# Performance work log

Measured on AMD Instinct MI355X. Metric: run time of the kernel, lower is better.

## Reference

```python
import jax, jax.numpy as jnp
import numpy as np

T, B, D_IN, NQ = 256, 2048, 128, 8  # time, batch, input_dim, n_qubits == hidden_dim


def setup_inputs() -> dict:
    key = jax.random.key(0)
    ks = jax.random.split(key, 13)
    s = 1.0 / np.sqrt(D_IN + NQ)
    def lin(ka, kb):
        W = jax.random.uniform(ka, (D_IN + NQ, NQ), jnp.float32, -s, s)
        b = jax.random.uniform(kb, (NQ,), jnp.float32, -s, s)
        return W, b
    Wf, bf = lin(ks[0], ks[1])
    Wi, bi = lin(ks[2], ks[3])
    Wg, bg = lin(ks[4], ks[5])
    Wo, bo = lin(ks[6], ks[7])
    # trainable RX angles per wire for each of the 4 quantum gates
    thf = jax.random.normal(ks[8], (NQ,), jnp.float32) * 0.1
    thi = jax.random.normal(ks[9], (NQ,), jnp.float32) * 0.1
    thg = jax.random.normal(ks[10], (NQ,), jnp.float32) * 0.1
    tho = jax.random.normal(ks[11], (NQ,), jnp.float32) * 0.1
    inputs = jax.random.normal(ks[12], (T, B, D_IN), jnp.float32)
    return {"inputs": inputs, "Wf": Wf, "bf": bf, "Wi": Wi, "bi": bi,
            "Wg": Wg, "bg": bg, "Wo": Wo, "bo": bo,
            "thf": thf, "thi": thi, "thg": thg, "tho": tho}


def _qgate(lin_out, theta):
    # |0..0> -> RX(x_i) encode -> RX(theta_i) trainable -> <PauliZ_i> = cos(x_i + theta_i)
    return jnp.cos(lin_out + theta)


def reference(inputs, Wf, bf, Wi, bi, Wg, bg, Wo, bo, thf, thi, thg, tho):
    Bsz = inputs.shape[1]
    h0 = jnp.zeros((Bsz, NQ), inputs.dtype)
    c0 = jnp.zeros((Bsz, NQ), inputs.dtype)

    def step(carry, x):
        hx, cx = carry
        comb = jnp.concatenate([x, hx], axis=1)  # [B, D_IN+NQ]
        f = jax.nn.sigmoid(_qgate(comb @ Wf + bf, thf))
        i = jax.nn.sigmoid(_qgate(comb @ Wi + bi, thi))
        g = jnp.tanh(_qgate(comb @ Wg + bg, thg))
        o = jax.nn.sigmoid(_qgate(comb @ Wo + bo, tho))
        cx = f * cx + i * g
        hx = o * jnp.tanh(cx)
        return (hx, cx), hx

    (hx, cx), outputs = jax.lax.scan(step, (h0, c0), inputs)
    return outputs, hx, cx
```

## Files before the change

### kernel.cpp

```cpp
#include <hip/hip_runtime.h>

#define T_DIM 256
#define B_DIM 2048
#define D_IN_DIM 128
#define NQ 8
#define ROWS_PER_BLK 64
#define XSTRIDE 129
#define TSTRIDE 33

__global__ __launch_bounds__(256) void qlstm_gemm(
    const float* __restrict__ X,
    const float* __restrict__ Wf, const float* __restrict__ Wi,
    const float* __restrict__ Wg, const float* __restrict__ Wo,
    const float* __restrict__ bf, const float* __restrict__ bi,
    const float* __restrict__ bg, const float* __restrict__ bo,
    const float* __restrict__ thf, const float* __restrict__ thi,
    const float* __restrict__ thg, const float* __restrict__ tho,
    float4* __restrict__ Z)
{
    __shared__ float xs[ROWS_PER_BLK * XSTRIDE];
    __shared__ float wsh[4 * D_IN_DIM * NQ];

    const int t = (int)threadIdx.x;
    const int r0 = (int)blockIdx.x * ROWS_PER_BLK;

    const int wid  = __builtin_amdgcn_readfirstlane(t >> 6);
    const int lane = t & 63;

    const float* W  = (wid == 0) ? Wf  : (wid == 1) ? Wi  : (wid == 2) ? Wg  : Wo;
    const float* BB = (wid == 0) ? bf  : (wid == 1) ? bi  : (wid == 2) ? bg  : bo;
    const float* TH = (wid == 0) ? thf : (wid == 1) ? thi : (wid == 2) ? thg : tho;

    {
        const float4* Wg4 = (const float4*)W;
        float4* wd = (float4*)&wsh[wid * (D_IN_DIM * NQ)];
#pragma unroll
        for (int j = 0; j < 4; j++) wd[j * 64 + lane] = Wg4[j * 64 + lane];
    }

    const float4* Xg = (const float4*)(X + (size_t)r0 * D_IN_DIM);
#pragma unroll
    for (int i = 0; i < 8; i++) {
        int L = t + i * 256;
        float4 v = Xg[L];
        int row = L >> 5;
        int k4  = L & 31;
        float* d = &xs[row * XSTRIDE + k4 * 4];
        d[0] = v.x; d[1] = v.y; d[2] = v.z; d[3] = v.w;
    }
    __syncthreads();

    float acc[NQ];
#pragma unroll
    for (int q = 0; q < NQ; q++) acc[q] = BB[q] + TH[q];

    const float*  xrow = &xs[lane * XSTRIDE];
    const float4* wk   = (const float4*)&wsh[wid * (D_IN_DIM * NQ)];
#pragma unroll 4
    for (int k = 0; k < D_IN_DIM; k++) {
        float xk = xrow[k];
        float4 wa = wk[2 * k];
        float4 wb = wk[2 * k + 1];
        acc[0] += xk * wa.x; acc[1] += xk * wa.y; acc[2] += xk * wa.z; acc[3] += xk * wa.w;
        acc[4] += xk * wb.x; acc[5] += xk * wb.y; acc[6] += xk * wb.z; acc[7] += xk * wb.w;
    }

    __syncthreads();
    float* tile = xs;
#pragma unroll
    for (int q = 0; q < NQ; q++)
        tile[lane * TSTRIDE + q * 4 + wid] = acc[q];
    __syncthreads();

    float4* Zblk = Z + (size_t)r0 * NQ;
#pragma unroll
    for (int i = 0; i < 2; i++) {
        int F = t + i * 256;
        int r = F >> 3, q = F & 7;
        const float* s = &tile[r * TSTRIDE + q * 4];
        Zblk[F] = make_float4(s[0], s[1], s[2], s[3]);
    }
}

#define INV_2PI 0.15915494309189535f
#define L2E     1.4426950408889634f

__device__ __forceinline__ float hw_cos(float x) {
    return __builtin_amdgcn_cosf(x * INV_2PI);
}
__device__ __forceinline__ float hw_tanh(float x) {
    return 1.0f - 2.0f * __builtin_amdgcn_rcpf(__builtin_amdgcn_exp2f((2.0f * L2E) * x) + 1.0f);
}

#define POLY_G(u) \
    fmaf((u), fmaf((u), fmaf((u), -0.027717f, 0.120472f), -0.331065f), 0.999904f)

#define BCAST8(x, J) \
    __int_as_float(__builtin_amdgcn_ds_swizzle(__float_as_int(x), ((J) << 5) | 0x18))

#define LSTM_STEP_R(zv, hdst) { \
    float h0 = BCAST8(h, 0), h1 = BCAST8(h, 1), h2 = BCAST8(h, 2), h3 = BCAST8(h, 3); \
    float h4 = BCAST8(h, 4), h5 = BCAST8(h, 5), h6 = BCAST8(h, 6), h7 = BCAST8(h, 7); \
    float f0 = fmaf(h0, whf[0], (zv).x), f1 = fmaf(h1, whf[1], 0.0f); \
    float i0 = fmaf(h0, whi[0], (zv).y), i1 = fmaf(h1, whi[1], 0.0f); \
    float g0 = fmaf(h0, whg[0], (zv).z), g1 = fmaf(h1, whg[1], 0.0f); \
    float o0 = fmaf(h0, who[0], (zv).w), o1 = fmaf(h1, who[1], 0.0f); \
    f0 = fmaf(h2, whf[2], f0); f1 = fmaf(h3, whf[3], f1); \
    i0 = fmaf(h2, whi[2], i0); i1 = fmaf(h3, whi[3], i1); \
    g0 = fmaf(h2, whg[2], g0); g1 = fmaf(h3, whg[3], g1); \
    o0 = fmaf(h2, who[2], o0); o1 = fmaf(h3, who[3], o1); \
    f0 = fmaf(h4, whf[4], f0); f1 = fmaf(h5, whf[5], f1); \
    i0 = fmaf(h4, whi[4], i0); i1 = fmaf(h5, whi[5], i1); \
    g0 = fmaf(h4, whg[4], g0); g1 = fmaf(h5, whg[5], g1); \
    o0 = fmaf(h4, who[4], o0); o1 = fmaf(h5, who[5], o1); \
    f0 = fmaf(h6, whf[6], f0); f1 = fmaf(h7, whf[7], f1); \
    i0 = fmaf(h6, whi[6], i0); i1 = fmaf(h7, whi[7], i1); \
    g0 = fmaf(h6, whg[6], g0); g1 = fmaf(h7, whg[7], g1); \
    o0 = fmaf(h6, who[6], o0); o1 = fmaf(h7, who[7], o1); \
    float tf = hw_cos(f0 + f1); \
    float ti = hw_cos(i0 + i1); \
    float tg = hw_cos(g0 + g1); \
    float to = hw_cos(o0 + o1); \
    float pf = POLY_G(0.25f * (tf * tf)); \
    float pi_ = POLY_G(0.25f * (ti * ti)); \
    float pg = POLY_G(tg * tg); \
    float po = POLY_G(0.25f * (to * to)); \
    float fg = fmaf(tf * pf, 0.25f, 0.5f); \
    float ig = fmaf(ti * pi_, 0.25f, 0.5f); \
    float gg = tg * pg; \
    float og = fmaf(to * po, 0.25f, 0.5f); \
    c = fmaf(fg, c, ig * gg); \
    h = og * hw_tanh(c); \
    (hdst) = h; }

__global__ __launch_bounds__(64) void qlstm_recur(
    const float4* __restrict__ Z,
    const float* __restrict__ Wf, const float* __restrict__ Wi,
    const float* __restrict__ Wg, const float* __restrict__ Wo,
    float* __restrict__ out,
    float* __restrict__ state,
    int t0, int ct, int first, int last)
{
    const int tid = (int)blockIdx.x * 64 + (int)threadIdx.x;
    const int q   = tid & 7;

    float whf[8], whi[8], whg[8], who[8];
#pragma unroll
    for (int j = 0; j < 8; j++) {
        whf[j] = Wf[(D_IN_DIM + j) * NQ + q];
        whi[j] = Wi[(D_IN_DIM + j) * NQ + q];
        whg[j] = Wg[(D_IN_DIM + j) * NQ + q];
        who[j] = Wo[(D_IN_DIM + j) * NQ + q];
    }

    float h, c;
    if (first) { h = 0.0f; c = 0.0f; }
    else       { h = state[tid]; c = state[B_DIM * NQ + tid]; }

    const size_t stepsz = (size_t)B_DIM * NQ;
    const float4* Zp = Z + tid;
    float* og_ptr = out + (size_t)t0 * stepsz + tid;

    float4 bufA[8], bufB[8];
    float houtA[8], houtB[8];
#pragma unroll
    for (int s = 0; s < 8; s++) bufA[s] = Zp[(size_t)s * stepsz];

    for (int tb = 0; tb < ct; tb += 16) {
#pragma unroll
        for (int s = 0; s < 8; s++) bufB[s] = Zp[(size_t)(tb + 8 + s) * stepsz];
        __builtin_amdgcn_sched_barrier(0);
#pragma unroll
        for (int s = 0; s < 8; s++) {
            float4 z = bufA[s];
            LSTM_STEP_R(z, houtA[s])
        }
        if (tb + 16 < ct) {
#pragma unroll
            for (int s = 0; s < 8; s++) bufA[s] = Zp[(size_t)(tb + 16 + s) * stepsz];
        }
        __builtin_amdgcn_sched_barrier(0);
#pragma unroll
        for (int s = 0; s < 8; s++) og_ptr[(size_t)s * stepsz] = houtA[s];
#pragma unroll
        for (int s = 0; s < 8; s++) {
            float4 z = bufB[s];
            LSTM_STEP_R(z, houtB[s])
        }
#pragma unroll
        for (int s = 0; s < 8; s++) og_ptr[(size_t)(8 + s) * stepsz] = houtB[s];
        og_ptr += (size_t)16 * stepsz;
    }

    if (last) {
        out[(size_t)T_DIM * stepsz + tid] = h;
        out[(size_t)T_DIM * stepsz + stepsz + tid] = c;
    } else {
        state[tid] = h;
        state[B_DIM * NQ + tid] = c;
    }
}

extern "C" void kernel_launch(void* const* d_in, const int* in_sizes, int n_in,
                              void* d_out, int out_size, void* d_ws, size_t ws_size,
                              hipStream_t stream) {
    const float* X   = (const float*)d_in[0];
    const float* Wf  = (const float*)d_in[1];
    const float* bf  = (const float*)d_in[2];
    const float* Wi  = (const float*)d_in[3];
    const float* bi  = (const float*)d_in[4];
    const float* Wg  = (const float*)d_in[5];
    const float* bg  = (const float*)d_in[6];
    const float* Wo  = (const float*)d_in[7];
    const float* bo  = (const float*)d_in[8];
    const float* thf = (const float*)d_in[9];
    const float* thi = (const float*)d_in[10];
    const float* thg = (const float*)d_in[11];
    const float* tho = (const float*)d_in[12];
    float* out = (float*)d_out;

    const size_t state_bytes = (size_t)2 * B_DIM * NQ * sizeof(float);
    float* state = (float*)d_ws;
    float4* Zbuf = (float4*)((char*)d_ws + state_bytes);
    size_t avail = ws_size > state_bytes ? ws_size - state_bytes : 0;
    const size_t z_bytes_per_t = (size_t)B_DIM * NQ * sizeof(float4);
    int maxChunkT = (int)(avail / z_bytes_per_t);
    if (maxChunkT > T_DIM) maxChunkT = T_DIM;
    maxChunkT &= ~15;
    if (maxChunkT < 16) maxChunkT = 16;

    int t0 = 0;
    int first = 1;
    while (t0 < T_DIM) {
        int ct = (T_DIM - t0 < maxChunkT) ? (T_DIM - t0) : maxChunkT;
        int rows = ct * B_DIM;
        qlstm_gemm<<<rows / ROWS_PER_BLK, 256, 0, stream>>>(
            X + (size_t)t0 * B_DIM * D_IN_DIM,
            Wf, Wi, Wg, Wo, bf, bi, bg, bo, thf, thi, thg, tho,
            Zbuf);
        int last = (t0 + ct == T_DIM) ? 1 : 0;
        qlstm_recur<<<(B_DIM * NQ) / 64, 64, 0, stream>>>(
            Zbuf, Wf, Wi, Wg, Wo, out, state, t0, ct, first, last);
        t0 += ct;
        first = 0;
    }
}
```

Measured before the change: 444.9 us.

## Process two rows per thread with float4 X loads in two K-passes

The input-projection GEMM kernel now handles 128 rows per block, and each thread computes two rows so every weight load from LDS is reused twice. X is staged as float4 in two half-K passes with a padded stride of 17, which allows vectorized LDS reads instead of scalar ones. This is meant to lower LDS traffic per FMA and halve the number of blocks. The cost is more registers per thread, an extra pair of barriers per pass, and fewer blocks to spread across CUs.

Result: no change. 451.9 us (+1.6%).

```diff
diff --git a/kernel.cpp b/kernel.cpp
--- a/kernel.cpp
+++ b/kernel.cpp
@@ -4,8 +4,8 @@
 #define B_DIM 2048
 #define D_IN_DIM 128
 #define NQ 8
-#define ROWS_PER_BLK 64
-#define XSTRIDE 129
+#define ROWS_PER_BLK 128
+#define S4 17
 #define TSTRIDE 33
 
 __global__ __launch_bounds__(256) void qlstm_gemm(
@@ -18,7 +18,7 @@
     const float* __restrict__ thg, const float* __restrict__ tho,
     float4* __restrict__ Z)
 {
-    __shared__ float xs[ROWS_PER_BLK * XSTRIDE];
+    __shared__ float4 xs4[ROWS_PER_BLK * S4];
     __shared__ float wsh[4 * D_IN_DIM * NQ];
 
     const int t = (int)threadIdx.x;
@@ -38,43 +38,71 @@
         for (int j = 0; j < 4; j++) wd[j * 64 + lane] = Wg4[j * 64 + lane];
     }
 
+    float acc0[NQ], acc1[NQ];
+#pragma unroll
+    for (int q = 0; q < NQ; q++) { float b0 = BB[q] + TH[q]; acc0[q] = b0; acc1[q] = b0; }
+
     const float4* Xg = (const float4*)(X + (size_t)r0 * D_IN_DIM);
-#pragma unroll
-    for (int i = 0; i < 8; i++) {
-        int L = t + i * 256;
-        float4 v = Xg[L];
-        int row = L >> 5;
-        int k4  = L & 31;
-        float* d = &xs[row * XSTRIDE + k4 * 4];
-        d[0] = v.x; d[1] = v.y; d[2] = v.z; d[3] = v.w;
-    }
+    const float4* wk = (const float4*)&wsh[wid * (D_IN_DIM * NQ)];
+
+#pragma unroll
+    for (int pass = 0; pass < 2; pass++) {
+        __syncthreads();
+#pragma unroll
+        for (int i = 0; i < 8; i++) {
+            int L = t + i * 256;
+            int row = L >> 4;
+            int c   = L & 15;
+            xs4[row * S4 + c] = Xg[(size_t)row * 32 + 16 * pass + c];
+        }
+        __syncthreads();
+
+        const float4* xr0 = &xs4[lane * S4];
+        const float4* xr1 = &xs4[(lane + 64) * S4];
+        const int wbase = 128 * pass;
+#pragma unroll 2
+        for (int kb = 0; kb < 16; kb++) {
+            float4 x0 = xr0[kb];
+            float4 x1 = xr1[kb];
+            float4 wa0 = wk[wbase + 8 * kb + 0], wb0 = wk[wbase + 8 * kb + 1];
+            float4 wa1 = wk[wbase + 8 * kb + 2], wb1 = wk[wbase + 8 * kb + 3];
+            float4 wa2 = wk[wbase + 8 * kb + 4], wb2 = wk[wbase + 8 * kb + 5];
+            float4 wa3 = wk[wbase + 8 * kb + 6], wb3 = wk[wbase + 8 * kb + 7];
+
+            acc0[0] += x0.x * wa0.x; acc0[1] += x0.x * wa0.y; acc0[2] += x0.x * wa0.z; acc0[3] += x0.x * wa0.w;
+            acc0[4] += x0.x * wb0.x; acc0[5] += x0.x * wb0.y; acc0[6] += x0.x * wb0.z; acc0[7] += x0.x * wb0.w;
+            acc1[0] += x1.x * wa0.x; acc1[1] += x1.x * wa0.y; acc1[2] += x1.x * wa0.z; acc1[3] += x1.x * wa0.w;
+            acc1[4] += x1.x * wb0.x; acc1[5] += x1.x * wb0.y; acc1[6] += x1.x * wb0.z; acc1[7] += x1.x * wb0.w;
+
+            acc0[0] += x0.y * wa1.x; acc0[1] += x0.y * wa1.y; acc0[2] += x0.y * wa1.z; acc0[3] += x0.y * wa1.w;
+            acc0[4] += x0.y * wb1.x; acc0[5] += x0.y * wb1.y; acc0[6] += x0.y * wb1.z; acc0[7] += x0.y * wb1.w;
+            acc1[0] += x1.y * wa1.x; acc1[1] += x1.y * wa1.y; acc1[2] += x1.y * wa1.z; acc1[3] += x1.y * wa1.w;
+            acc1[4] += x1.y * wb1.x; acc1[5] += x1.y * wb1.y; acc1[6] += x1.y * wb1.z; acc1[7] += x1.y * wb1.w;
+
+            acc0[0] += x0.z * wa2.x; acc0[1] += x0.z * wa2.y; acc0[2] += x0.z * wa2.z; acc0[3] += x0.z * wa2.w;
+            acc0[4] += x0.z * wb2.x; acc0[5] += x0.z * wb2.y; acc0[6] += x0.z * wb2.z; acc0[7] += x0.z * wb2.w;
+            acc1[0] += x1.z * wa2.x; acc1[1] += x1.z * wa2.y; acc1[2] += x1.z * wa2.z; acc1[3] += x1.z * wa2.w;
+            acc1[4] += x1.z * wb2.x; acc1[5] += x1.z * wb2.y; acc1[6] += x1.z * wb2.z; acc1[7] += x1.z * wb2.w;
+
+            acc0[0] += x0.w * wa3.x; acc0[1] += x0.w * wa3.y; acc0[2] += x0.w * wa3.z; acc0[3] += x0.w * wa3.w;
+            acc0[4] += x0.w * wb3.x; acc0[5] += x0.w * wb3.y; acc0[6] += x0.w * wb3.z; acc0[7] += x0.w * wb3.w;
+            acc1[0] += x1.w * wa3.x; acc1[1] += x1.w * wa3.y; acc1[2] += x1.w * wa3.z; acc1[3] += x1.w * wa3.w;
+            acc1[4] += x1.w * wb3.x; acc1[5] += x1.w * wb3.y; acc1[6] += x1.w * wb3.z; acc1[7] += x1.w * wb3.w;
+        }
+    }
+
     __syncthreads();
-
-    float acc[NQ];
-#pragma unroll
-    for (int q = 0; q < NQ; q++) acc[q] = BB[q] + TH[q];
-
-    const float*  xrow = &xs[lane * XSTRIDE];
-    const float4* wk   = (const float4*)&wsh[wid * (D_IN_DIM * NQ)];
-#pragma unroll 4
-    for (int k = 0; k < D_IN_DIM; k++) {
-        float xk = xrow[k];
-        float4 wa = wk[2 * k];
-        float4 wb = wk[2 * k + 1];
-        acc[0] += xk * wa.x; acc[1] += xk * wa.y; acc[2] += xk * wa.z; acc[3] += xk * wa.w;
-        acc[4] += xk * wb.x; acc[5] += xk * wb.y; acc[6] += xk * wb.z; acc[7] += xk * wb.w;
-    }
-
+    float* tile = (float*)xs4;
+#pragma unroll
+    for (int q = 0; q < NQ; q++) {
+        tile[lane * TSTRIDE + q * 4 + wid] = acc0[q];
+        tile[(lane + 64) * TSTRIDE + q * 4 + wid] = acc1[q];
+    }
     __syncthreads();
-    float* tile = xs;
-#pragma unroll
-    for (int q = 0; q < NQ; q++)
-        tile[lane * TSTRIDE + q * 4 + wid] = acc[q];
-    __syncthreads();
 
     float4* Zblk = Z + (size_t)r0 * NQ;
 #pragma unroll
-    for (int i = 0; i < 2; i++) {
+    for (int i = 0; i < 4; i++) {
         int F = t + i * 256;
         int r = F >> 3, q = F & 7;
         const float* s = &tile[r * TSTRIDE + q * 4];
```

## Compute input projection GEMM with bf16 MFMA instead of FP32 FMAs

Applied to the files above, without the earlier changes.

Converts X and the gate weights to bf16 in LDS and computes the 64x32 projection per block with mfma_f32_16x16x32_bf16, adding bias plus theta at the output stage. This targets the scalar FMA cost of the input projection kernel. The recurrent kernel, likely the dominant cost, is unchanged. Precision drops to bf16 inputs, which may hurt accuracy against the fp32 reference.

Result: no change. 440.1 us (-1.1%).

```diff
diff --git a/kernel.cpp b/kernel.cpp
--- a/kernel.cpp
+++ b/kernel.cpp
@@ -5,8 +5,18 @@
 #define D_IN_DIM 128
 #define NQ 8
 #define ROWS_PER_BLK 64
-#define XSTRIDE 129
+#define XR 136
+#define WR 136
 #define TSTRIDE 33
+
+typedef __attribute__((ext_vector_type(8))) short bf16x8;
+typedef __attribute__((ext_vector_type(4))) float f32x4;
+
+__device__ __forceinline__ ushort f2bf(float x) {
+    union { float f; unsigned u; } a; a.f = x;
+    unsigned r = a.u + 0x7fff + ((a.u >> 16) & 1);
+    return (ushort)(r >> 16);
+}
 
 __global__ __launch_bounds__(256) void qlstm_gemm(
     const float* __restrict__ X,
@@ -18,24 +28,34 @@
     const float* __restrict__ thg, const float* __restrict__ tho,
     float4* __restrict__ Z)
 {
-    __shared__ float xs[ROWS_PER_BLK * XSTRIDE];
-    __shared__ float wsh[4 * D_IN_DIM * NQ];
+    __shared__ ushort xlds[ROWS_PER_BLK * XR];
+    __shared__ ushort wt[32 * WR];
+    __shared__ float bsh[32];
 
     const int t = (int)threadIdx.x;
     const int r0 = (int)blockIdx.x * ROWS_PER_BLK;
-
     const int wid  = __builtin_amdgcn_readfirstlane(t >> 6);
     const int lane = t & 63;
 
-    const float* W  = (wid == 0) ? Wf  : (wid == 1) ? Wi  : (wid == 2) ? Wg  : Wo;
-    const float* BB = (wid == 0) ? bf  : (wid == 1) ? bi  : (wid == 2) ? bg  : bo;
-    const float* TH = (wid == 0) ? thf : (wid == 1) ? thi : (wid == 2) ? thg : tho;
-
     {
+        const float* W = (wid == 0) ? Wf : (wid == 1) ? Wi : (wid == 2) ? Wg : Wo;
         const float4* Wg4 = (const float4*)W;
-        float4* wd = (float4*)&wsh[wid * (D_IN_DIM * NQ)];
-#pragma unroll
-        for (int j = 0; j < 4; j++) wd[j * 64 + lane] = Wg4[j * 64 + lane];
+#pragma unroll
+        for (int j = 0; j < 4; j++) {
+            int i = j * 64 + lane;
+            float4 v = Wg4[i];
+            int k = i >> 1, q0 = (i & 1) * 4;
+            wt[((q0 + 0) * 4 + wid) * WR + k] = f2bf(v.x);
+            wt[((q0 + 1) * 4 + wid) * WR + k] = f2bf(v.y);
+            wt[((q0 + 2) * 4 + wid) * WR + k] = f2bf(v.z);
+            wt[((q0 + 3) * 4 + wid) * WR + k] = f2bf(v.w);
+        }
+    }
+    if (t < 32) {
+        int gate = t & 3, q = t >> 2;
+        const float* bb = (gate == 0) ? bf  : (gate == 1) ? bi  : (gate == 2) ? bg  : bo;
+        const float* th = (gate == 0) ? thf : (gate == 1) ? thi : (gate == 2) ? thg : tho;
+        bsh[t] = bb[q] + th[q];
     }
 
     const float4* Xg = (const float4*)(X + (size_t)r0 * D_IN_DIM);
@@ -44,32 +64,38 @@
         int L = t + i * 256;
         float4 v = Xg[L];
         int row = L >> 5;
-        int k4  = L & 31;
-        float* d = &xs[row * XSTRIDE + k4 * 4];
-        d[0] = v.x; d[1] = v.y; d[2] = v.z; d[3] = v.w;
+        int k4  = (L & 31) * 4;
+        ushort4 p;
+        p.x = f2bf(v.x); p.y = f2bf(v.y); p.z = f2bf(v.z); p.w = f2bf(v.w);
+        *(ushort4*)&xlds[row * XR + k4] = p;
     }
     __syncthreads();
 
-    float acc[NQ];
-#pragma unroll
-    for (int q = 0; q < NQ; q++) acc[q] = BB[q] + TH[q];
-
-    const float*  xrow = &xs[lane * XSTRIDE];
-    const float4* wk   = (const float4*)&wsh[wid * (D_IN_DIM * NQ)];
-#pragma unroll 4
-    for (int k = 0; k < D_IN_DIM; k++) {
-        float xk = xrow[k];
-        float4 wa = wk[2 * k];
-        float4 wb = wk[2 * k + 1];
-        acc[0] += xk * wa.x; acc[1] += xk * wa.y; acc[2] += xk * wa.z; acc[3] += xk * wa.w;
-        acc[4] += xk * wb.x; acc[5] += xk * wb.y; acc[6] += xk * wb.z; acc[7] += xk * wb.w;
-    }
-
+    const int band = wid * 16;
+    const int arow = band + (lane & 15);
+    const int koff = (lane >> 4) * 8;
+    f32x4 d0 = {0.f, 0.f, 0.f, 0.f};
+    f32x4 d1 = {0.f, 0.f, 0.f, 0.f};
+#pragma unroll
+    for (int kt = 0; kt < 4; kt++) {
+        bf16x8 a  = *(const bf16x8*)&xlds[arow * XR + kt * 32 + koff];
+        bf16x8 b0 = *(const bf16x8*)&wt[(lane & 15) * WR + kt * 32 + koff];
+        bf16x8 b1 = *(const bf16x8*)&wt[(16 + (lane & 15)) * WR + kt * 32 + koff];
+        d0 = __builtin_amdgcn_mfma_f32_16x16x32_bf16(a, b0, d0, 0, 0, 0);
+        d1 = __builtin_amdgcn_mfma_f32_16x16x32_bf16(a, b1, d1, 0, 0, 0);
+    }
     __syncthreads();
-    float* tile = xs;
-#pragma unroll
-    for (int q = 0; q < NQ; q++)
-        tile[lane * TSTRIDE + q * 4 + wid] = acc[q];
+
+    float* tile = (float*)xlds;
+    {
+        int drow = band + (lane >> 4) * 4;
+        int c = lane & 15;
+#pragma unroll
+        for (int r = 0; r < 4; r++) {
+            tile[(drow + r) * TSTRIDE + c]      = d0[r];
+            tile[(drow + r) * TSTRIDE + 16 + c] = d1[r];
+        }
+    }
     __syncthreads();
 
     float4* Zblk = Z + (size_t)r0 * NQ;
@@ -78,7 +104,8 @@
         int F = t + i * 256;
         int r = F >> 3, q = F & 7;
         const float* s = &tile[r * TSTRIDE + q * 4];
-        Zblk[F] = make_float4(s[0], s[1], s[2], s[3]);
+        Zblk[F] = make_float4(s[0] + bsh[q * 4 + 0], s[1] + bsh[q * 4 + 1],
+                              s[2] + bsh[q * 4 + 2], s[3] + bsh[q * 4 + 3]);
     }
 }
 
```
